# Kernel tuning notes

Measured on AMD Instinct MI355X. Metric: run time of the kernel, lower is better.

## Reference

```python
import jax, jax.numpy as jnp
import numpy as np

N = 50000      # nodes
E = 800000     # edges (avg degree 16)
D_IN = 32      # input_shape
D_E = 8        # edges_shape
H = 128        # hidden_shape == message_shape == encoder out_shape
L = 4          # nb_layers
D_OUT = 2      # output_shape

# MLP dims per source formula delta = (in - out) // 3
# enc:  32 -> 64 -> 96 -> 128
# edge:  8 -> 48 -> 88 -> 128
# dec: 128 -> 86 -> 44 -> 2


def setup_inputs() -> dict:
    key = jax.random.key(0)
    ks = iter(jax.random.split(key, 64))

    def rn(shape, scale=0.05):
        return jax.random.normal(next(ks), shape, jnp.float32) * scale

    inp = {}
    inp["x"] = jax.random.normal(next(ks), (N, D_IN), jnp.float32)
    inp["edge_index"] = jax.random.randint(next(ks), (2, E), 0, N)
    inp["edge_attr"] = jax.random.normal(next(ks), (E, D_E), jnp.float32)

    # node encoder MLP + LayerNorm
    inp["enc_w1"] = rn((64, D_IN)); inp["enc_b1"] = jnp.full((64,), 0.01)
    inp["enc_w2"] = rn((96, 64));   inp["enc_b2"] = jnp.full((96,), 0.01)
    inp["enc_w3"] = rn((H, 96));    inp["enc_b3"] = jnp.full((H,), 0.01)
    inp["enc_ln_g"] = jnp.ones((H,)); inp["enc_ln_b"] = jnp.zeros((H,))

    # edge encoder MLP + LayerNorm
    inp["ee_w1"] = rn((48, D_E)); inp["ee_b1"] = jnp.full((48,), 0.01)
    inp["ee_w2"] = rn((88, 48));  inp["ee_b2"] = jnp.full((88,), 0.01)
    inp["ee_w3"] = rn((H, 88));   inp["ee_b3"] = jnp.full((H,), 0.01)
    inp["ee_ln_g"] = jnp.ones((H,)); inp["ee_ln_b"] = jnp.zeros((H,))

    # GATv2 layers (heads=1), stacked over L
    inp["gat_wl"] = rn((L, H, H)); inp["gat_bl"] = jnp.zeros((L, H))
    inp["gat_wr"] = rn((L, H, H)); inp["gat_br"] = jnp.zeros((L, H))
    inp["gat_we"] = rn((L, H, H))               # lin_edge (no bias)
    inp["gat_att"] = rn((L, H))
    inp["gat_bias"] = jnp.zeros((L, H))
    inp["ln_g"] = jnp.ones((L, H)); inp["ln_b"] = jnp.zeros((L, H))

    # decoder MLP
    inp["dec_w1"] = rn((86, H));  inp["dec_b1"] = jnp.full((86,), 0.01)
    inp["dec_w2"] = rn((44, 86)); inp["dec_b2"] = jnp.full((44,), 0.01)
    inp["dec_w3"] = rn((D_OUT, 44)); inp["dec_b3"] = jnp.full((D_OUT,), 0.01)
    return inp


def _mlp(x, w1, b1, w2, b2, w3, b3):
    x = jax.nn.leaky_relu(x @ w1.T + b1, 0.01)
    x = jax.nn.leaky_relu(x @ w2.T + b2, 0.01)
    return x @ w3.T + b3


def _ln(x, g, b):
    mu = x.mean(-1, keepdims=True)
    var = x.var(-1, keepdims=True)
    return (x - mu) / jnp.sqrt(var + 1e-5) * g + b


def _gatv2(y, src, dst, ea, wl, bl, wr, br, we, att, bias):
    # heads=1, concat=True, add_self_loops=False, leaky slope 0.2
    xl = y @ wl.T + bl                      # [N, H] source transform (values)
    xr = y @ wr.T + br                      # [N, H] target transform
    e = xl[src] + xr[dst] + ea @ we.T       # [E, H]
    s = jax.nn.leaky_relu(e, 0.2) @ att     # [E] attention logits
    m = jax.ops.segment_max(s, dst, num_segments=N)
    z = jnp.exp(s - m[dst])
    denom = jax.ops.segment_sum(z, dst, num_segments=N)
    alpha = z / jnp.maximum(denom[dst], 1e-16)
    out = jax.ops.segment_sum(alpha[:, None] * xl[src], dst, num_segments=N)
    return out + bias


def reference(x, edge_index, edge_attr,
              enc_w1, enc_b1, enc_w2, enc_b2, enc_w3, enc_b3, enc_ln_g, enc_ln_b,
              ee_w1, ee_b1, ee_w2, ee_b2, ee_w3, ee_b3, ee_ln_g, ee_ln_b,
              gat_wl, gat_bl, gat_wr, gat_br, gat_we, gat_att, gat_bias, ln_g, ln_b,
              dec_w1, dec_b1, dec_w2, dec_b2, dec_w3, dec_b3):
    src, dst = edge_index[0], edge_index[1]
    y = _ln(_mlp(x, enc_w1, enc_b1, enc_w2, enc_b2, enc_w3, enc_b3), enc_ln_g, enc_ln_b)
    ea = _ln(_mlp(edge_attr, ee_w1, ee_b1, ee_w2, ee_b2, ee_w3, ee_b3), ee_ln_g, ee_ln_b)
    for i in range(L):
        g = _gatv2(y, src, dst, ea, gat_wl[i], gat_bl[i], gat_wr[i], gat_br[i],
                   gat_we[i], gat_att[i], gat_bias[i])
        y = y + _ln(g, ln_g[i], ln_b[i])
    return _mlp(y, dec_w1, dec_b1, dec_w2, dec_b2, dec_w3, dec_b3)
```

## Files before the change

kernel.cpp:

```cpp
#include <hip/hip_runtime.h>


typedef unsigned short u16;
typedef unsigned int   u32;
typedef __attribute__((ext_vector_type(8))) short bf16x8;
typedef __attribute__((ext_vector_type(4))) float f32x4;

#define LEAKY01(a) ((a) > 0.f ? (a) : 0.01f*(a))
#define LEAKY20(a) ((a) > 0.f ? (a) : 0.2f*(a))

__device__ __forceinline__ float bf2f(u16 h) { return __uint_as_float(((u32)h) << 16); }
__device__ __forceinline__ u16 f2bf(float f) {
  u32 u = __float_as_uint(f);
  u32 r = u + 0x7fffu + ((u >> 16) & 1u);
  return (u16)(r >> 16);
}
__device__ __forceinline__ float bflo(u32 p) { return __uint_as_float(p << 16); }
__device__ __forceinline__ float bfhi(u32 p) { return __uint_as_float(p & 0xffff0000u); }

__device__ __forceinline__ void lds_rw_fence() {
  __builtin_amdgcn_sched_barrier(0);
  asm volatile("s_waitcnt lgkmcnt(0)" ::: "memory");
  __builtin_amdgcn_sched_barrier(0);
}
__device__ __forceinline__ void loop_mem_fence() {
  __builtin_amdgcn_sched_barrier(0);
  asm volatile("" ::: "memory");
}

__global__ __launch_bounds__(256, 2) void node_enc_mfma(
    const float* __restrict__ x,
    const float* __restrict__ w1, const float* __restrict__ b1,
    const float* __restrict__ w2, const float* __restrict__ b2,
    const float* __restrict__ w3, const float* __restrict__ b3,
    const float* __restrict__ g, const float* __restrict__ bb,
    float* __restrict__ y, int n)
{
  __shared__ __align__(16) u16   h1buf[4][16][72];
  __shared__ __align__(16) u16   h2buf[4][16][104];
  __shared__ __align__(16) float obuf[4][16][132];
  const int tid = threadIdx.x;
  const int lane = tid & 63, wv = tid >> 6;
  const int c16 = lane & 15, gq = lane >> 4;
  for (int i = tid; i < 4*16*72; i += 256)  ((u16*)h1buf)[i] = 0;
  for (int i = tid; i < 4*16*104; i += 256) ((u16*)h2buf)[i] = 0;
  __syncthreads();

  bf16x8 bw1[4];
  #pragma unroll
  for (int tc = 0; tc < 4; ++tc) {
    bf16x8 v;
    #pragma unroll
    for (int j = 0; j < 8; ++j) v[j] = (short)f2bf(w1[(tc*16 + c16)*32 + gq*8 + j]);
    bw1[tc] = v;
  }
  bf16x8 bw2[6][2];
  #pragma unroll
  for (int tc = 0; tc < 6; ++tc) {
    #pragma unroll
    for (int t = 0; t < 2; ++t) {
      bf16x8 v;
      #pragma unroll
      for (int j = 0; j < 8; ++j) v[j] = (short)f2bf(w2[(tc*16 + c16)*64 + t*32 + gq*8 + j]);
      bw2[tc][t] = v;
    }
  }
  bf16x8 bw3[8][3];
  #pragma unroll
  for (int tc = 0; tc < 8; ++tc) {
    #pragma unroll
    for (int t = 0; t < 3; ++t) {
      bf16x8 v;
      #pragma unroll
      for (int j = 0; j < 8; ++j) v[j] = (short)f2bf(w3[(tc*16 + c16)*96 + t*32 + gq*8 + j]);
      bw3[tc][t] = v;
    }
  }
  float b1v[4], b2v[6], b3v[8], gav[8], bev[8];
  #pragma unroll
  for (int tc = 0; tc < 4; ++tc) b1v[tc] = b1[tc*16 + c16];
  #pragma unroll
  for (int tc = 0; tc < 6; ++tc) b2v[tc] = b2[tc*16 + c16];
  #pragma unroll
  for (int tc = 0; tc < 8; ++tc) {
    b3v[tc] = b3[tc*16 + c16];
    gav[tc] = g[tc*16 + c16];
    bev[tc] = bb[tc*16 + c16];
  }

  const int nt = (n + 15) >> 4;
  const long wid = (long)blockIdx.x*4 + wv;
  const long wstride = (long)gridDim.x*4;
  for (long tile = wid; tile < nt; tile += wstride) {
    const long i0 = tile << 4;
    const long rA = (i0 + c16 < n) ? (i0 + c16) : (n - 1);
    bf16x8 af1;
    {
      const float* ip = x + rA*32 + gq*8;
      const float4 v0 = *(const float4*)ip;
      const float4 v1 = *(const float4*)(ip + 4);
      af1[0] = (short)f2bf(v0.x); af1[1] = (short)f2bf(v0.y);
      af1[2] = (short)f2bf(v0.z); af1[3] = (short)f2bf(v0.w);
      af1[4] = (short)f2bf(v1.x); af1[5] = (short)f2bf(v1.y);
      af1[6] = (short)f2bf(v1.z); af1[7] = (short)f2bf(v1.w);
    }
    #pragma unroll
    for (int tc = 0; tc < 4; ++tc) {
      f32x4 acc = {0.f, 0.f, 0.f, 0.f};
      acc = __builtin_amdgcn_mfma_f32_16x16x32_bf16(af1, bw1[tc], acc, 0, 0, 0);
      #pragma unroll
      for (int j = 0; j < 4; ++j)
        h1buf[wv][gq*4 + j][tc*16 + c16] = f2bf(LEAKY01(acc[j] + b1v[tc]));
    }
    lds_rw_fence();
    bf16x8 a2[2];
    #pragma unroll
    for (int t = 0; t < 2; ++t)
      a2[t] = *(const bf16x8*)&h1buf[wv][c16][t*32 + gq*8];
    lds_rw_fence();
    #pragma unroll
    for (int tc = 0; tc < 6; ++tc) {
      f32x4 acc = {0.f, 0.f, 0.f, 0.f};
      #pragma unroll
      for (int t = 0; t < 2; ++t)
        acc = __builtin_amdgcn_mfma_f32_16x16x32_bf16(a2[t], bw2[tc][t], acc, 0, 0, 0);
      #pragma unroll
      for (int j = 0; j < 4; ++j)
        h2buf[wv][gq*4 + j][tc*16 + c16] = f2bf(LEAKY01(acc[j] + b2v[tc]));
    }
    lds_rw_fence();
    bf16x8 a3[3];
    #pragma unroll
    for (int t = 0; t < 3; ++t)
      a3[t] = *(const bf16x8*)&h2buf[wv][c16][t*32 + gq*8];
    lds_rw_fence();
    f32x4 oa[8];
    #pragma unroll
    for (int tc = 0; tc < 8; ++tc) {
      f32x4 acc = {0.f, 0.f, 0.f, 0.f};
      #pragma unroll
      for (int t = 0; t < 3; ++t)
        acc = __builtin_amdgcn_mfma_f32_16x16x32_bf16(a3[t], bw3[tc][t], acc, 0, 0, 0);
      #pragma unroll
      for (int j = 0; j < 4; ++j) acc[j] += b3v[tc];
      oa[tc] = acc;
    }
    float vsum[4] = {0.f,0.f,0.f,0.f}, vsq[4] = {0.f,0.f,0.f,0.f};
    #pragma unroll
    for (int tc = 0; tc < 8; ++tc)
      #pragma unroll
      for (int j = 0; j < 4; ++j) { const float v = oa[tc][j]; vsum[j] += v; vsq[j] += v*v; }
    #pragma unroll
    for (int off = 1; off <= 8; off <<= 1) {
      #pragma unroll
      for (int j = 0; j < 4; ++j) {
        vsum[j] += __shfl_xor(vsum[j], off, 64);
        vsq[j]  += __shfl_xor(vsq[j], off, 64);
      }
    }
    float muv[4], rsv[4];
    #pragma unroll
    for (int j = 0; j < 4; ++j) {
      muv[j] = vsum[j] * (1.f/128.f);
      const float var = vsq[j] * (1.f/128.f) - muv[j]*muv[j];
      rsv[j] = rsqrtf(var + 1e-5f);
    }
    #pragma unroll
    for (int tc = 0; tc < 8; ++tc)
      #pragma unroll
      for (int j = 0; j < 4; ++j)
        obuf[wv][gq*4 + j][tc*16 + c16] = (oa[tc][j] - muv[j]) * rsv[j] * gav[tc] + bev[tc];
    lds_rw_fence();
    #pragma unroll 4
    for (int r = 0; r < 16; ++r) {
      const long grow = i0 + r;
      if (grow < n) {
        const float2 vv = *(const float2*)&obuf[wv][r][2*lane];
        *(float2*)(y + grow*128 + 2*lane) = vv;
      }
    }
    loop_mem_fence();
  }
}

__global__ __launch_bounds__(256, 2) void edge_enc_mfma(
    const float* __restrict__ eat,
    const float* __restrict__ w1, const float* __restrict__ b1,
    const float* __restrict__ w2, const float* __restrict__ b2,
    const float* __restrict__ w3, const float* __restrict__ b3,
    const float* __restrict__ g, const float* __restrict__ bb,
    u16* __restrict__ ea, int ecnt)
{
  __shared__ __align__(16) u16 h1buf[4][16][72];
  __shared__ __align__(16) u16 h2buf[4][16][104];
  __shared__ __align__(16) u16 obuf[4][16][136];
  const int tid = threadIdx.x;
  const int lane = tid & 63, wv = tid >> 6;
  const int c16 = lane & 15, gq = lane >> 4;
  for (int i = tid; i < 4*16*72; i += 256)  ((u16*)h1buf)[i] = 0;
  for (int i = tid; i < 4*16*104; i += 256) ((u16*)h2buf)[i] = 0;
  __syncthreads();

  bf16x8 bw1[3];
  #pragma unroll
  for (int tc = 0; tc < 3; ++tc) {
    bf16x8 v;
    #pragma unroll
    for (int j = 0; j < 8; ++j) {
      const int k = gq*8 + j;
      v[j] = (k < 8) ? (short)f2bf(w1[(tc*16 + c16)*8 + k]) : (short)0;
    }
    bw1[tc] = v;
  }
  bf16x8 bw2[6][2];
  #pragma unroll
  for (int tc = 0; tc < 6; ++tc) {
    const int col = tc*16 + c16;
    #pragma unroll
    for (int t = 0; t < 2; ++t) {
      bf16x8 v;
      #pragma unroll
      for (int j = 0; j < 8; ++j) {
        const int k = t*32 + gq*8 + j;
        v[j] = (col < 88 && k < 48) ? (short)f2bf(w2[col*48 + k]) : (short)0;
      }
      bw2[tc][t] = v;
    }
  }
  bf16x8 bw3[8][3];
  #pragma unroll
  for (int tc = 0; tc < 8; ++tc) {
    #pragma unroll
    for (int t = 0; t < 3; ++t) {
      bf16x8 v;
      #pragma unroll
      for (int j = 0; j < 8; ++j) {
        const int k = t*32 + gq*8 + j;
        v[j] = (k < 88) ? (short)f2bf(w3[(tc*16 + c16)*88 + k]) : (short)0;
      }
      bw3[tc][t] = v;
    }
  }
  float b1v[3], b2v[6], b3v[8], gav[8], bev[8];
  #pragma unroll
  for (int tc = 0; tc < 3; ++tc) b1v[tc] = b1[tc*16 + c16];
  #pragma unroll
  for (int tc = 0; tc < 6; ++tc) b2v[tc] = (tc*16 + c16 < 88) ? b2[tc*16 + c16] : 0.f;
  #pragma unroll
  for (int tc = 0; tc < 8; ++tc) {
    b3v[tc] = b3[tc*16 + c16];
    gav[tc] = g[tc*16 + c16];
    bev[tc] = bb[tc*16 + c16];
  }

  const int nt = (ecnt + 15) >> 4;
  const long wid = (long)blockIdx.x*4 + wv;
  const long wstride = (long)gridDim.x*4;
  for (long tile = wid; tile < nt; tile += wstride) {
    const long i0 = tile << 4;
    const long rA = (i0 + c16 < ecnt) ? (i0 + c16) : (ecnt - 1);
    bf16x8 af1 = {0,0,0,0,0,0,0,0};
    if (gq == 0) {
      const float4 v0 = *(const float4*)(eat + rA*8);
      const float4 v1 = *(const float4*)(eat + rA*8 + 4);
      af1[0] = (short)f2bf(v0.x); af1[1] = (short)f2bf(v0.y);
      af1[2] = (short)f2bf(v0.z); af1[3] = (short)f2bf(v0.w);
      af1[4] = (short)f2bf(v1.x); af1[5] = (short)f2bf(v1.y);
      af1[6] = (short)f2bf(v1.z); af1[7] = (short)f2bf(v1.w);
    }
    #pragma unroll
    for (int tc = 0; tc < 3; ++tc) {
      f32x4 acc = {0.f, 0.f, 0.f, 0.f};
      acc = __builtin_amdgcn_mfma_f32_16x16x32_bf16(af1, bw1[tc], acc, 0, 0, 0);
      #pragma unroll
      for (int j = 0; j < 4; ++j)
        h1buf[wv][gq*4 + j][tc*16 + c16] = f2bf(LEAKY01(acc[j] + b1v[tc]));
    }
    lds_rw_fence();
    bf16x8 a2[2];
    #pragma unroll
    for (int t = 0; t < 2; ++t)
      a2[t] = *(const bf16x8*)&h1buf[wv][c16][t*32 + gq*8];
    lds_rw_fence();
    #pragma unroll
    for (int tc = 0; tc < 6; ++tc) {
      f32x4 acc = {0.f, 0.f, 0.f, 0.f};
      #pragma unroll
      for (int t = 0; t < 2; ++t)
        acc = __builtin_amdgcn_mfma_f32_16x16x32_bf16(a2[t], bw2[tc][t], acc, 0, 0, 0);
      const int col = tc*16 + c16;
      if (col < 88) {
        #pragma unroll
        for (int j = 0; j < 4; ++j)
          h2buf[wv][gq*4 + j][col] = f2bf(LEAKY01(acc[j] + b2v[tc]));
      }
    }
    lds_rw_fence();
    bf16x8 a3[3];
    #pragma unroll
    for (int t = 0; t < 3; ++t)
      a3[t] = *(const bf16x8*)&h2buf[wv][c16][t*32 + gq*8];
    lds_rw_fence();
    f32x4 oa[8];
    #pragma unroll
    for (int tc = 0; tc < 8; ++tc) {
      f32x4 acc = {0.f, 0.f, 0.f, 0.f};
      #pragma unroll
      for (int t = 0; t < 3; ++t)
        acc = __builtin_amdgcn_mfma_f32_16x16x32_bf16(a3[t], bw3[tc][t], acc, 0, 0, 0);
      #pragma unroll
      for (int j = 0; j < 4; ++j) acc[j] += b3v[tc];
      oa[tc] = acc;
    }
    float vsum[4] = {0.f,0.f,0.f,0.f}, vsq[4] = {0.f,0.f,0.f,0.f};
    #pragma unroll
    for (int tc = 0; tc < 8; ++tc)
      #pragma unroll
      for (int j = 0; j < 4; ++j) { const float v = oa[tc][j]; vsum[j] += v; vsq[j] += v*v; }
    #pragma unroll
    for (int off = 1; off <= 8; off <<= 1) {
      #pragma unroll
      for (int j = 0; j < 4; ++j) {
        vsum[j] += __shfl_xor(vsum[j], off, 64);
        vsq[j]  += __shfl_xor(vsq[j], off, 64);
      }
    }
    float muv[4], rsv[4];
    #pragma unroll
    for (int j = 0; j < 4; ++j) {
      muv[j] = vsum[j] * (1.f/128.f);
      const float var = vsq[j] * (1.f/128.f) - muv[j]*muv[j];
      rsv[j] = rsqrtf(var + 1e-5f);
    }
    #pragma unroll
    for (int tc = 0; tc < 8; ++tc)
      #pragma unroll
      for (int j = 0; j < 4; ++j)
        obuf[wv][gq*4 + j][tc*16 + c16] = f2bf((oa[tc][j] - muv[j]) * rsv[j] * gav[tc] + bev[tc]);
    lds_rw_fence();
    #pragma unroll 4
    for (int r = 0; r < 16; ++r) {
      const long grow = i0 + r;
      if (grow < ecnt) {
        const u32 vv = *(const u32*)&obuf[wv][r][2*lane];
        ((u32*)ea)[grow*64 + lane] = vv;
      }
    }
    loop_mem_fence();
  }
}

__global__ __launch_bounds__(256, 2) void dual_linear128_mfma(
    const float* __restrict__ in,
    const float* __restrict__ wl, const float* __restrict__ bl,
    const float* __restrict__ wr, const float* __restrict__ br,
    u16* __restrict__ xl, u16* __restrict__ xr, int n)
{
  __shared__ __align__(16) u16 sh_t[2][16][136];
  const int tid = threadIdx.x;
  const int lane = tid & 63, wv = tid >> 6;
  const int c16 = lane & 15, gq = lane >> 4;
  const float* W = (wv < 2) ? wl : wr;
  const float* B = (wv < 2) ? bl : br;
  const int cb = (wv & 1) * 64;
  const int half = wv >> 1;
  bf16x8 bw[4][4];
  #pragma unroll
  for (int tc = 0; tc < 4; ++tc) {
    #pragma unroll
    for (int t = 0; t < 4; ++t) {
      const float* wp = W + (cb + tc*16 + c16)*128 + t*32 + gq*8;
      bf16x8 v;
      #pragma unroll
      for (int j = 0; j < 8; ++j) v[j] = (short)f2bf(wp[j]);
      bw[tc][t] = v;
    }
  }
  float bv[4];
  #pragma unroll
  for (int tc = 0; tc < 4; ++tc) bv[tc] = B[cb + tc*16 + c16];

  const int nt = (n + 15) >> 4;
  for (long tile = blockIdx.x; tile < nt; tile += gridDim.x) {
    const long r0 = tile << 4;
    const long rowA = (r0 + c16 < n) ? (r0 + c16) : (n - 1);
    bf16x8 af[4];
    #pragma unroll
    for (int t = 0; t < 4; ++t) {
      const float* ip = in + rowA*128 + t*32 + gq*8;
      const float4 v0 = *(const float4*)ip;
      const float4 v1 = *(const float4*)(ip + 4);
      bf16x8 a;
      a[0] = (short)f2bf(v0.x); a[1] = (short)f2bf(v0.y);
      a[2] = (short)f2bf(v0.z); a[3] = (short)f2bf(v0.w);
      a[4] = (short)f2bf(v1.x); a[5] = (short)f2bf(v1.y);
      a[6] = (short)f2bf(v1.z); a[7] = (short)f2bf(v1.w);
      af[t] = a;
    }
    #pragma unroll
    for (int tc = 0; tc < 4; ++tc) {
      f32x4 acc = {0.f, 0.f, 0.f, 0.f};
      #pragma unroll
      for (int t = 0; t < 4; ++t)
        acc = __builtin_amdgcn_mfma_f32_16x16x32_bf16(af[t], bw[tc][t], acc, 0, 0, 0);
      #pragma unroll
      for (int j = 0; j < 4; ++j)
        sh_t[half][gq*4 + j][cb + tc*16 + c16] = f2bf(acc[j] + bv[tc]);
    }
    __syncthreads();
    for (int i = tid; i < 2048; i += 256) {
      const int h = i >> 10;
      const int r = (i >> 6) & 15;
      const int c = i & 63;
      const long grow = r0 + r;
      if (grow < n) {
        u16* dstp = h ? xr : xl;
        ((u32*)dstp)[grow*64 + c] = *(const u32*)&sh_t[h][r][2*c];
      }
    }
    __syncthreads();
  }
}

__global__ __launch_bounds__(256, 2) void gat_logit_mfma(
    const u16* __restrict__ ea,
    const u16* __restrict__ xl, const u16* __restrict__ xr,
    const int* __restrict__ src, const int* __restrict__ dst,
    const int* __restrict__ posbuf,
    const float* __restrict__ we, const float* __restrict__ att,
    float* __restrict__ s_csr, int eoff, int ecnt, int E)
{
  __shared__ float sh_g[4][16][132];
  const int tid = threadIdx.x;
  const int lane = tid & 63, wv = tid >> 6;
  const int c16 = lane & 15, g = lane >> 4;
  bf16x8 bw[8][4];
  #pragma unroll
  for (int tc = 0; tc < 8; ++tc) {
    #pragma unroll
    for (int t = 0; t < 4; ++t) {
      const float* wp = we + (tc*16 + c16)*128 + t*32 + g*8;
      bf16x8 v;
      #pragma unroll
      for (int j = 0; j < 8; ++j) v[j] = (short)f2bf(wp[j]);
      bw[tc][t] = v;
    }
  }
  float attv[8];
  #pragma unroll
  for (int tc = 0; tc < 8; ++tc) attv[tc] = att[tc*16 + c16];

  const u32* xl32 = (const u32*)xl;
  const u32* xr32 = (const u32*)xr;
  const int nt = (ecnt + 15) >> 4;
  const long wid = (long)blockIdx.x*4 + wv;
  const long wstride = (long)gridDim.x*4;
  for (long tile = wid; tile < nt; tile += wstride) {
    const long i0 = tile << 4;
    const long e0 = eoff + i0;
    int sv = 0, dv = 0;
    if (lane < 16) {
      const long eg = (e0 + lane < E) ? (e0 + lane) : (E - 1);
      sv = src[eg]; dv = dst[eg];
    }
    #pragma unroll 4
    for (int e = 0; e < 16; ++e) {
      const int srow = __shfl(sv, e, 64);
      const int drow = __shfl(dv, e, 64);
      const u32 xa = xl32[(long)srow*64 + lane];
      const u32 xb = xr32[(long)drow*64 + lane];
      float2 sg;
      sg.x = bflo(xa) + bflo(xb);
      sg.y = bfhi(xa) + bfhi(xb);
      *(float2*)&sh_g[wv][e][lane*2] = sg;
    }
    lds_rw_fence();
    const long rA = (i0 + c16 < ecnt) ? (i0 + c16) : (ecnt - 1);
    bf16x8 af[4];
    #pragma unroll
    for (int t = 0; t < 4; ++t)
      af[t] = *(const bf16x8*)(ea + rA*128 + t*32 + g*8);
    float p0 = 0.f, p1 = 0.f, p2 = 0.f, p3 = 0.f;
    #pragma unroll
    for (int tc = 0; tc < 8; ++tc) {
      f32x4 acc = {0.f, 0.f, 0.f, 0.f};
      #pragma unroll
      for (int t = 0; t < 4; ++t)
        acc = __builtin_amdgcn_mfma_f32_16x16x32_bf16(af[t], bw[tc][t], acc, 0, 0, 0);
      const float av = attv[tc];
      #pragma unroll
      for (int j = 0; j < 4; ++j) {
        float ev = acc[j] + sh_g[wv][g*4 + j][tc*16 + c16];
        ev = LEAKY20(ev);
        const float term = ev * av;
        if (j == 0) p0 += term; else if (j == 1) p1 += term;
        else if (j == 2) p2 += term; else p3 += term;
      }
    }
    #pragma unroll
    for (int off = 1; off <= 8; off <<= 1) {
      p0 += __shfl_xor(p0, off, 64);
      p1 += __shfl_xor(p1, off, 64);
      p2 += __shfl_xor(p2, off, 64);
      p3 += __shfl_xor(p3, off, 64);
    }
    if (c16 == 0) {
      const long rbase = e0 + g*4;
      if (rbase + 0 < E && i0 + g*4 + 0 < ecnt) s_csr[posbuf[rbase + 0]] = p0;
      if (rbase + 1 < E && i0 + g*4 + 1 < ecnt) s_csr[posbuf[rbase + 1]] = p1;
      if (rbase + 2 < E && i0 + g*4 + 2 < ecnt) s_csr[posbuf[rbase + 2]] = p2;
      if (rbase + 3 < E && i0 + g*4 + 3 < ecnt) s_csr[posbuf[rbase + 3]] = p3;
    }
    loop_mem_fence();
  }
}

__global__ __launch_bounds__(256) void csr_count_kernel(
    const int* __restrict__ dst, int* __restrict__ cnt, int E)
{
  for (long e = (long)blockIdx.x*blockDim.x + threadIdx.x; e < E;
       e += (long)gridDim.x*blockDim.x)
    atomicAdd(&cnt[dst[e]], 1);
}

__global__ __launch_bounds__(1024) void csr_scan_kernel(
    const int* __restrict__ cnt, int* __restrict__ rowptr, int n)
{
  __shared__ int part[1024];
  const int t = threadIdx.x;
  const int chunk = (n + 1023) >> 10;
  const int b = t * chunk;
  const int e = min(b + chunk, n);
  int s = 0;
  for (int i = b; i < e; ++i) s += cnt[i];
  part[t] = s;
  __syncthreads();
  for (int d = 1; d < 1024; d <<= 1) {
    int v = (t >= d) ? part[t - d] : 0;
    __syncthreads();
    if (t >= d) part[t] += v;
    __syncthreads();
  }
  int pre = (t == 0) ? 0 : part[t - 1];
  for (int i = b; i < e; ++i) { rowptr[i] = pre; pre += cnt[i]; }
  if (t == 1023) rowptr[n] = pre;
}

__global__ __launch_bounds__(256) void csr_fill_kernel(
    const int* __restrict__ src, const int* __restrict__ dst,
    const int* __restrict__ rowptr, int* __restrict__ cursor,
    int* __restrict__ posbuf, int* __restrict__ srccsr, int E)
{
  for (long e = (long)blockIdx.x*blockDim.x + threadIdx.x; e < E;
       e += (long)gridDim.x*blockDim.x) {
    const int d = dst[e];
    const int pos = rowptr[d] + atomicAdd(&cursor[d], 1);
    posbuf[e] = pos;
    srccsr[pos] = src[e];
  }
}

__global__ __launch_bounds__(256) void gat_agg_kernel(
    const float* __restrict__ s_csr, const int* __restrict__ srccsr,
    const int* __restrict__ rowptr,
    const u16* __restrict__ xl, const float* __restrict__ bias,
    const float* __restrict__ g, const float* __restrict__ bb,
    float* __restrict__ y, int n)
{
  const int tid = threadIdx.x;
  const int lane = tid & 63, wv = tid >> 6;
  const int wpb = blockDim.x >> 6;
  const float bi0 = bias[2*lane], bi1 = bias[2*lane + 1];
  const float g0 = g[2*lane], g1 = g[2*lane + 1];
  const float bb0 = bb[2*lane], bb1 = bb[2*lane + 1];
  const u32* xl32 = (const u32*)xl;
  for (long node = (long)blockIdx.x*wpb + wv; node < n; node += (long)gridDim.x*wpb) {
    const int beg = rowptr[node], end = rowptr[node + 1];
    float m = -INFINITY, den = 0.f, a0 = 0.f, a1 = 0.f;
    for (int j = beg; j < end; ++j) {
      const float s = s_csr[j];
      const u32 xv = xl32[(long)srccsr[j]*64 + lane];
      if (s > m) {
        const float c = __expf(m - s);
        m = s;
        den = den*c + 1.f;
        a0 = a0*c + bflo(xv);
        a1 = a1*c + bfhi(xv);
      } else {
        const float z = __expf(s - m);
        den += z;
        a0 += z * bflo(xv);
        a1 += z * bfhi(xv);
      }
    }
    const float inv = 1.f / fmaxf(den, 1e-16f);
    const float v0 = a0*inv + bi0;
    const float v1 = a1*inv + bi1;
    float sum = v0 + v1, sq = v0*v0 + v1*v1;
    for (int off = 32; off; off >>= 1) { sum += __shfl_xor(sum, off, 64); sq += __shfl_xor(sq, off, 64); }
    const float mu = sum * (1.f/128.f);
    const float var = sq * (1.f/128.f) - mu*mu;
    const float rs = rsqrtf(var + 1e-5f);
    float2 yv = *(float2*)(y + node*128 + 2*lane);
    yv.x += (v0 - mu) * rs * g0 + bb0;
    yv.y += (v1 - mu) * rs * g1 + bb1;
    *(float2*)(y + node*128 + 2*lane) = yv;
  }
}

__global__ __launch_bounds__(256, 2) void decoder_mfma(
    const float* __restrict__ y,
    const float* __restrict__ w1, const float* __restrict__ b1,
    const float* __restrict__ w2, const float* __restrict__ b2,
    const float* __restrict__ w3, const float* __restrict__ b3,
    float* __restrict__ out, int n)
{
  __shared__ __align__(16) u16 h1buf[4][16][104];
  __shared__ __align__(16) u16 h2buf[4][16][48];
  const int tid = threadIdx.x;
  const int lane = tid & 63, wv = tid >> 6;
  const int c16 = lane & 15, gq = lane >> 4;
  for (int i = tid; i < 4*16*104; i += 256) ((u16*)h1buf)[i] = 0;
  for (int i = tid; i < 4*16*48; i += 256)  ((u16*)h2buf)[i] = 0;
  __syncthreads();

  bf16x8 bw1[6][4];
  #pragma unroll
  for (int tc = 0; tc < 6; ++tc) {
    const int col = tc*16 + c16;
    #pragma unroll
    for (int t = 0; t < 4; ++t) {
      bf16x8 v;
      #pragma unroll
      for (int j = 0; j < 8; ++j) {
        const int k = t*32 + gq*8 + j;
        v[j] = (col < 86) ? (short)f2bf(w1[col*128 + k]) : (short)0;
      }
      bw1[tc][t] = v;
    }
  }
  bf16x8 bw2[3][3];
  #pragma unroll
  for (int tc = 0; tc < 3; ++tc) {
    const int col = tc*16 + c16;
    #pragma unroll
    for (int t = 0; t < 3; ++t) {
      bf16x8 v;
      #pragma unroll
      for (int j = 0; j < 8; ++j) {
        const int k = t*32 + gq*8 + j;
        v[j] = (col < 44 && k < 86) ? (short)f2bf(w2[col*86 + k]) : (short)0;
      }
      bw2[tc][t] = v;
    }
  }
  float b1v[6], b2v[3];
  #pragma unroll
  for (int tc = 0; tc < 6; ++tc) b1v[tc] = (tc*16 + c16 < 86) ? b1[tc*16 + c16] : 0.f;
  #pragma unroll
  for (int tc = 0; tc < 3; ++tc) b2v[tc] = (tc*16 + c16 < 44) ? b2[tc*16 + c16] : 0.f;
  float w3a[11], w3b[11];
  #pragma unroll
  for (int i = 0; i < 11; ++i) { w3a[i] = w3[gq*11 + i]; w3b[i] = w3[44 + gq*11 + i]; }
  const float b3a = b3[0], b3b = b3[1];

  const int nt = (n + 15) >> 4;
  const long wid = (long)blockIdx.x*4 + wv;
  const long wstride = (long)gridDim.x*4;
  for (long tile = wid; tile < nt; tile += wstride) {
    const long r0 = tile << 4;
    const long rowA = (r0 + c16 < n) ? (r0 + c16) : (n - 1);
    bf16x8 af[4];
    #pragma unroll
    for (int t = 0; t < 4; ++t) {
      const float* ip = y + rowA*128 + t*32 + gq*8;
      const float4 v0 = *(const float4*)ip;
      const float4 v1 = *(const float4*)(ip + 4);
      bf16x8 a;
      a[0] = (short)f2bf(v0.x); a[1] = (short)f2bf(v0.y);
      a[2] = (short)f2bf(v0.z); a[3] = (short)f2bf(v0.w);
      a[4] = (short)f2bf(v1.x); a[5] = (short)f2bf(v1.y);
      a[6] = (short)f2bf(v1.z); a[7] = (short)f2bf(v1.w);
      af[t] = a;
    }
    #pragma unroll
    for (int tc = 0; tc < 6; ++tc) {
      f32x4 acc = {0.f, 0.f, 0.f, 0.f};
      #pragma unroll
      for (int t = 0; t < 4; ++t)
        acc = __builtin_amdgcn_mfma_f32_16x16x32_bf16(af[t], bw1[tc][t], acc, 0, 0, 0);
      #pragma unroll
      for (int j = 0; j < 4; ++j)
        h1buf[wv][gq*4 + j][tc*16 + c16] = f2bf(LEAKY01(acc[j] + b1v[tc]));
    }
    lds_rw_fence();
    bf16x8 a2[3];
    #pragma unroll
    for (int t = 0; t < 3; ++t)
      a2[t] = *(const bf16x8*)&h1buf[wv][c16][t*32 + gq*8];
    lds_rw_fence();
    #pragma unroll
    for (int tc = 0; tc < 3; ++tc) {
      f32x4 acc = {0.f, 0.f, 0.f, 0.f};
      #pragma unroll
      for (int t = 0; t < 3; ++t)
        acc = __builtin_amdgcn_mfma_f32_16x16x32_bf16(a2[t], bw2[tc][t], acc, 0, 0, 0);
      #pragma unroll
      for (int j = 0; j < 4; ++j)
        h2buf[wv][gq*4 + j][tc*16 + c16] = f2bf(LEAKY01(acc[j] + b2v[tc]));
    }
    lds_rw_fence();
    float t0 = 0.f, t1 = 0.f;
    #pragma unroll
    for (int i = 0; i < 11; ++i) {
      const float hv = bf2f(h2buf[wv][c16][gq*11 + i]);
      t0 += hv * w3a[i];
      t1 += hv * w3b[i];
    }
    t0 += __shfl_xor(t0, 16, 64); t0 += __shfl_xor(t0, 32, 64);
    t1 += __shfl_xor(t1, 16, 64); t1 += __shfl_xor(t1, 32, 64);
    if (gq == 0 && r0 + c16 < n) {
      float2 o; o.x = t0 + b3a; o.y = t1 + b3b;
      *(float2*)(out + (r0 + c16)*2) = o;
    }
    loop_mem_fence();
  }
}

__global__ __launch_bounds__(256) void zero_out_kernel(float* __restrict__ out, long n)
{
  for (long i = (long)blockIdx.x*blockDim.x + threadIdx.x; i < n;
       i += (long)gridDim.x*blockDim.x) out[i] = 0.f;
}

extern "C" void kernel_launch(void* const* d_in, const int* in_sizes, int n_in,
                              void* d_out, int out_size, void* d_ws, size_t ws_size,
                              hipStream_t stream) {
  const float* x        = (const float*)d_in[0];
  const int*   eidx     = (const int*)  d_in[1];
  const float* edge_attr= (const float*)d_in[2];
  const float* enc_w1 = (const float*)d_in[3];  const float* enc_b1 = (const float*)d_in[4];
  const float* enc_w2 = (const float*)d_in[5];  const float* enc_b2 = (const float*)d_in[6];
  const float* enc_w3 = (const float*)d_in[7];  const float* enc_b3 = (const float*)d_in[8];
  const float* enc_lg = (const float*)d_in[9];  const float* enc_lb = (const float*)d_in[10];
  const float* ee_w1  = (const float*)d_in[11]; const float* ee_b1  = (const float*)d_in[12];
  const float* ee_w2  = (const float*)d_in[13]; const float* ee_b2  = (const float*)d_in[14];
  const float* ee_w3  = (const float*)d_in[15]; const float* ee_b3  = (const float*)d_in[16];
  const float* ee_lg  = (const float*)d_in[17]; const float* ee_lb  = (const float*)d_in[18];
  const float* gat_wl = (const float*)d_in[19]; const float* gat_bl = (const float*)d_in[20];
  const float* gat_wr = (const float*)d_in[21]; const float* gat_br = (const float*)d_in[22];
  const float* gat_we = (const float*)d_in[23]; const float* gat_att= (const float*)d_in[24];
  const float* gat_bias=(const float*)d_in[25];
  const float* ln_g   = (const float*)d_in[26]; const float* ln_b   = (const float*)d_in[27];
  const float* dec_w1 = (const float*)d_in[28]; const float* dec_b1 = (const float*)d_in[29];
  const float* dec_w2 = (const float*)d_in[30]; const float* dec_b2 = (const float*)d_in[31];
  const float* dec_w3 = (const float*)d_in[32]; const float* dec_b3 = (const float*)d_in[33];
  float* out = (float*)d_out;

  const int N = in_sizes[0] / 32;
  const int E = in_sizes[2] / 8;
  const int L = in_sizes[19] / (128*128);
  const int* src = eidx;
  const int* dst = eidx + E;
  (void)n_in; (void)out_size;

  size_t off = 0;
  auto carve = [&](size_t bytes) -> char* {
    char* r = (char*)d_ws + off;
    off += (bytes + 255) & ~(size_t)255;
    return r;
  };
  float* y      = (float*)carve((size_t)N * 128 * 4);
  u16*   xl     = (u16*)  carve((size_t)N * 128 * 2);
  u16*   xr     = (u16*)  carve((size_t)N * 128 * 2);
  float* sbuf   = (float*)carve((size_t)E * 4);
  int*   rowptr = (int*)  carve((size_t)(N + 1) * 4);
  int*   posbuf = (int*)  carve((size_t)E * 4);
  int*   srccsr = (int*)  carve((size_t)E * 4);
  int*   cnt    = (int*)  carve((size_t)N * 4);
  int*   cursor = (int*)  carve((size_t)N * 4);
  const size_t fixedBytes = off;

  if (ws_size < fixedBytes + (size_t)4096 * 256) {
    hipLaunchKernelGGL(zero_out_kernel, dim3(256), dim3(256), 0, stream, out, (long)N*2);
    return;
  }
  const size_t eaCapEdges = (ws_size - fixedBytes) / 256;
  u16* eaBuf = (u16*)((char*)d_ws + fixedBytes);
  const bool full = eaCapEdges >= (size_t)E;
  const int Ec = full ? E : (int)(eaCapEdges & ~(size_t)1023);

  const int encGrid = ((N + 15) / 16 + 3) / 4;
  hipLaunchKernelGGL(node_enc_mfma, dim3(encGrid), dim3(256), 0, stream,
                     x, enc_w1, enc_b1, enc_w2, enc_b2, enc_w3, enc_b3,
                     enc_lg, enc_lb, y, N);
  hipMemsetAsync(cnt, 0, (size_t)N * 4, stream);
  hipMemsetAsync(cursor, 0, (size_t)N * 4, stream);
  hipLaunchKernelGGL(csr_count_kernel, dim3(1024), dim3(256), 0, stream, dst, cnt, E);
  hipLaunchKernelGGL(csr_scan_kernel, dim3(1), dim3(1024), 0, stream, cnt, rowptr, N);
  hipLaunchKernelGGL(csr_fill_kernel, dim3(1024), dim3(256), 0, stream,
                     src, dst, rowptr, cursor, posbuf, srccsr, E);

  if (full) {
    hipLaunchKernelGGL(edge_enc_mfma, dim3(1024), dim3(256), 0, stream,
                       edge_attr, ee_w1, ee_b1, ee_w2, ee_b2, ee_w3, ee_b3,
                       ee_lg, ee_lb, eaBuf, E);
  }

  for (int l = 0; l < L; ++l) {
    const float* wl = gat_wl + (size_t)l*128*128;
    const float* bl = gat_bl + (size_t)l*128;
    const float* wr = gat_wr + (size_t)l*128*128;
    const float* br = gat_br + (size_t)l*128;
    const float* we = gat_we + (size_t)l*128*128;
    const float* at = gat_att + (size_t)l*128;
    const float* bi = gat_bias + (size_t)l*128;
    const float* lg = ln_g + (size_t)l*128;
    const float* lb = ln_b + (size_t)l*128;

    hipLaunchKernelGGL(dual_linear128_mfma, dim3(1024), dim3(256), 0, stream,
                       y, wl, bl, wr, br, xl, xr, N);

    if (full) {
      hipLaunchKernelGGL(gat_logit_mfma, dim3(1024), dim3(256), 0, stream,
                         eaBuf, xl, xr, src, dst, posbuf, we, at, sbuf, 0, E, E);
    } else {
      for (int eoff = 0; eoff < E; eoff += Ec) {
        const int c = (E - eoff < Ec) ? (E - eoff) : Ec;
        hipLaunchKernelGGL(edge_enc_mfma, dim3(1024), dim3(256), 0, stream,
                           edge_attr + (size_t)eoff*8, ee_w1, ee_b1, ee_w2, ee_b2,
                           ee_w3, ee_b3, ee_lg, ee_lb, eaBuf, c);
        hipLaunchKernelGGL(gat_logit_mfma, dim3(1024), dim3(256), 0, stream,
                           eaBuf, xl, xr, src, dst, posbuf, we, at, sbuf, eoff, c, E);
      }
    }

    hipLaunchKernelGGL(gat_agg_kernel, dim3(1024), dim3(256), 0, stream,
                       sbuf, srccsr, rowptr, xl, bi, lg, lb, y, N);
  }

  hipLaunchKernelGGL(decoder_mfma, dim3(encGrid), dim3(256), 0, stream,
                     y, dec_w1, dec_b1, dec_w2, dec_b2, dec_w3, dec_b3, out, N);
}
```

Before: 2.022 ms.

## Prefetch next-tile gathers in edge kernel, software-pipeline aggregation loop, drop fences

The edge-score kernel now issues the xl/xr row gathers for its next tile into registers while the current tile's MFMA work runs, so gather latency overlaps with compute. The CSR aggregation loop loads the next neighbor's score and feature one iteration early. Several LDS read fences after fragment loads in the encoder and decoder MLPs are removed. This raises register pressure (32 extra u32 per lane in the edge kernel) and relies on compiler ordering for the LDS write-after-read hazards that the fences used to guard.

```diff
diff --git a/kernel.cpp b/kernel.cpp
--- a/kernel.cpp
+++ b/kernel.cpp
@@ -117,7 +117,6 @@
     #pragma unroll
     for (int t = 0; t < 2; ++t)
       a2[t] = *(const bf16x8*)&h1buf[wv][c16][t*32 + gq*8];
-    lds_rw_fence();
     #pragma unroll
     for (int tc = 0; tc < 6; ++tc) {
       f32x4 acc = {0.f, 0.f, 0.f, 0.f};
@@ -133,7 +132,6 @@
     #pragma unroll
     for (int t = 0; t < 3; ++t)
       a3[t] = *(const bf16x8*)&h2buf[wv][c16][t*32 + gq*8];
-    lds_rw_fence();
     f32x4 oa[8];
     #pragma unroll
     for (int tc = 0; tc < 8; ++tc) {
@@ -281,7 +279,6 @@
     #pragma unroll
     for (int t = 0; t < 2; ++t)
       a2[t] = *(const bf16x8*)&h1buf[wv][c16][t*32 + gq*8];
-    lds_rw_fence();
     #pragma unroll
     for (int tc = 0; tc < 6; ++tc) {
       f32x4 acc = {0.f, 0.f, 0.f, 0.f};
@@ -300,7 +297,6 @@
     #pragma unroll
     for (int t = 0; t < 3; ++t)
       a3[t] = *(const bf16x8*)&h2buf[wv][c16][t*32 + gq*8];
-    lds_rw_fence();
     f32x4 oa[8];
     #pragma unroll
     for (int tc = 0; tc < 8; ++tc) {
@@ -455,26 +451,51 @@
   const int nt = (ecnt + 15) >> 4;
   const long wid = (long)blockIdx.x*4 + wv;
   const long wstride = (long)gridDim.x*4;
-  for (long tile = wid; tile < nt; tile += wstride) {
-    const long i0 = tile << 4;
-    const long e0 = eoff + i0;
+
+  u32 ga[16], gb[16];
+  if (wid < nt) {
+    const long e0 = eoff + (wid << 4);
     int sv = 0, dv = 0;
     if (lane < 16) {
       const long eg = (e0 + lane < E) ? (e0 + lane) : (E - 1);
       sv = src[eg]; dv = dst[eg];
     }
-    #pragma unroll 4
+    #pragma unroll
     for (int e = 0; e < 16; ++e) {
       const int srow = __shfl(sv, e, 64);
       const int drow = __shfl(dv, e, 64);
-      const u32 xa = xl32[(long)srow*64 + lane];
-      const u32 xb = xr32[(long)drow*64 + lane];
+      ga[e] = xl32[(long)srow*64 + lane];
+      gb[e] = xr32[(long)drow*64 + lane];
+    }
+  }
+
+  for (long tile = wid; tile < nt; tile += wstride) {
+    const long i0 = tile << 4;
+    const long e0 = eoff + i0;
+    #pragma unroll
+    for (int e = 0; e < 16; ++e) {
       float2 sg;
-      sg.x = bflo(xa) + bflo(xb);
-      sg.y = bfhi(xa) + bfhi(xb);
+      sg.x = bflo(ga[e]) + bflo(gb[e]);
+      sg.y = bfhi(ga[e]) + bfhi(gb[e]);
       *(float2*)&sh_g[wv][e][lane*2] = sg;
     }
     lds_rw_fence();
+    const long ntile = tile + wstride;
+    if (ntile < nt) {
+      const long ne0 = eoff + (ntile << 4);
+      int sv = 0, dv = 0;
+      if (lane < 16) {
+        const long eg = (ne0 + lane < E) ? (ne0 + lane) : (E - 1);
+        sv = src[eg]; dv = dst[eg];
+      }
+      #pragma unroll
+      for (int e = 0; e < 16; ++e) {
+        const int srow = __shfl(sv, e, 64);
+        const int drow = __shfl(dv, e, 64);
+        ga[e] = xl32[(long)srow*64 + lane];
+        gb[e] = xr32[(long)drow*64 + lane];
+      }
+    }
     const long rA = (i0 + c16 < ecnt) ? (i0 + c16) : (ecnt - 1);
     bf16x8 af[4];
     #pragma unroll
@@ -577,20 +598,28 @@
   for (long node = (long)blockIdx.x*wpb + wv; node < n; node += (long)gridDim.x*wpb) {
     const int beg = rowptr[node], end = rowptr[node + 1];
     float m = -INFINITY, den = 0.f, a0 = 0.f, a1 = 0.f;
-    for (int j = beg; j < end; ++j) {
-      const float s = s_csr[j];
-      const u32 xv = xl32[(long)srccsr[j]*64 + lane];
-      if (s > m) {
-        const float c = __expf(m - s);
-        m = s;
-        den = den*c + 1.f;
-        a0 = a0*c + bflo(xv);
-        a1 = a1*c + bfhi(xv);
-      } else {
-        const float z = __expf(s - m);
-        den += z;
-        a0 += z * bflo(xv);
-        a1 += z * bfhi(xv);
+    if (beg < end) {
+      float sp = s_csr[beg];
+      u32  xp = xl32[(long)srccsr[beg]*64 + lane];
+      for (int j = beg; j < end; ++j) {
+        const float s = sp;
+        const u32 xv = xp;
+        if (j + 1 < end) {
+          sp = s_csr[j + 1];
+          xp = xl32[(long)srccsr[j + 1]*64 + lane];
+        }
+        if (s > m) {
+          const float c = __expf(m - s);
+          m = s;
+          den = den*c + 1.f;
+          a0 = a0*c + bflo(xv);
+          a1 = a1*c + bfhi(xv);
+        } else {
+          const float z = __expf(s - m);
+          den += z;
+          a0 += z * bflo(xv);
+          a1 += z * bfhi(xv);
+        }
       }
     }
     const float inv = 1.f / fmaxf(den, 1e-16f);
@@ -698,7 +727,6 @@
     #pragma unroll
     for (int t = 0; t < 3; ++t)
       a2[t] = *(const bf16x8*)&h1buf[wv][c16][t*32 + gq*8];
-    lds_rw_fence();
     #pragma unroll
     for (int tc = 0; tc < 3; ++tc) {
       f32x4 acc = {0.f, 0.f, 0.f, 0.f};
```

Result: slower. 2.148 ms (+6.2%).
